# Optimization experiments

Hardware: AMD Instinct MI355X
Metric: run time of the kernel (lower is better)

The kernel has to match this reference:

```python
import jax, jax.numpy as jnp
import numpy as np

B, A, STATE_LEN, H, REL_LEN, E = 32, 64, 256, 128, 64, 16

def _mlp2(x, w1, b1, w2, b2):
    # DI-engine MLP, 2 layers, ReLU after every layer (incl. output)
    return jax.nn.relu(jax.nn.relu(x @ w1 + b1) @ w2 + b2)

def setup_inputs() -> dict:
    key = jax.random.key(0)
    ks = jax.random.split(key, 16)
    def w(k, fi, fo):
        return (jax.random.normal(k, (fi, fo), jnp.float32) / np.float32(np.sqrt(fi)))
    z = lambda n: jnp.zeros((n,), jnp.float32)
    return {
        "states": jax.random.normal(ks[0], (B, A, STATE_LEN), jnp.float32),
        "relations": jax.random.normal(ks[1], (B, A, A, REL_LEN), jnp.float32),
        "alive_mask": (jax.random.uniform(ks[2], (B, A)) > 0.3).astype(jnp.float32),
        "se_w1": w(ks[3], STATE_LEN, H), "se_b1": z(H),
        "se_w2": w(ks[4], H, H), "se_b2": z(H),
        "re_w1": w(ks[5], H + REL_LEN, H), "re_b1": z(H),
        "re_w2": w(ks[6], H, 2 * H), "re_b2": z(2 * H),
        "ra_w": w(ks[7], 3 * H, H), "ra_b": z(H),
        "ae_w1": w(ks[8], 4 * H, H), "ae_b1": z(H),
        "ae_w2": w(ks[9], H, 2 * H), "ae_b2": z(2 * H),
        "action_embed": jax.random.normal(ks[10], (E, H), jnp.float32) * np.float32(np.sqrt(2.0 / H)),
        "action_mask": jnp.ones((B, A, E + A), jnp.int32),
        "action": jax.random.randint(ks[11], (B,), 0, E + A),
        "agent_id": 0,
    }

def reference(states, relations, alive_mask,
              se_w1, se_b1, se_w2, se_b2,
              re_w1, re_b1, re_w2, re_b2,
              ra_w, ra_b,
              ae_w1, ae_b1, ae_w2, ae_b2,
              action_embed, action_mask, action, agent_id):
    del action_mask  # read by the torch module but never used
    b, a = states.shape[0], states.shape[1]
    h, e = se_w2.shape[1], action_embed.shape[0]
    # encode per-agent state: [B,A,H]
    s = _mlp2(states, se_w1, se_b1, se_w2, se_b2)
    # relation encoder: concat target-agent state onto each relation edge
    rel_in = jnp.concatenate(
        [relations, jnp.broadcast_to(s[:, None], (b, a, a, h))], axis=-1)
    r = _mlp2(rel_in, re_w1, re_b1, re_w2, re_b2)               # [B,A,A,2H]
    # relation aggregator: masked mean / masked max over source agents
    r_avr, r_max = jnp.split(r, 2, axis=-1)
    m = alive_mask[:, None, :, None]                             # [B,1,A,1]
    r_avr = (r_avr * m).mean(axis=-2)                            # [B,A,H]
    r_max = (r_max * m).max(axis=-2)                             # [B,A,H]
    s = jax.nn.relu(jnp.concatenate([s, r_avr, r_max], axis=-1) @ ra_w + ra_b)
    # pairwise action embeddings: [B,A,A,2H]
    ae_in = jnp.concatenate(
        [r,
         jnp.broadcast_to(s[:, None], (b, a, a, h)),
         jnp.broadcast_to(s[:, :, None], (b, a, a, h))], axis=-1)
    ae = _mlp2(ae_in, ae_w1, ae_b1, ae_w2, ae_b2)
    active, passive = jnp.split(ae, 2, axis=-1)                  # [B,A,A,H] each
    # acting agent `agent_id`: candidates = [embed_num self actions | A targeted actions]
    active_i = active[:, agent_id]                               # [B,A,H]
    active_full = jnp.concatenate(
        [jnp.broadcast_to(action_embed[None], (b, e, h)), active_i], axis=1)  # [B,E+A,H]
    sel = jnp.take_along_axis(active_full, action[:, None, None], axis=1)     # [B,1,H]
    state = s.at[:, agent_id].add(sel[:, 0])
    # passive side: target j receives passive embed iff action == E + j, else zero
    passive_i = passive[:, agent_id]                             # [B,A,H]
    hit = (action[:, None] == (e + jnp.arange(a))[None, :])      # [B,A]
    passive_sel = jnp.where(hit[:, :, None], passive_i, jnp.zeros((), states.dtype))
    state = state + passive_sel
    return state, sel[:, :, None], passive_sel
```

## Files before the change

### kernel.cpp

```cpp
#include <hip/hip_runtime.h>

#define NB 32
#define NA 64
#define SLEN 256
#define NH 128
#define RLEN 64
#define NE 16

typedef _Float16 f16;
typedef _Float16 f16x8 __attribute__((ext_vector_type(8)));
typedef _Float16 f16x4 __attribute__((ext_vector_type(4)));
typedef float f32x4 __attribute__((ext_vector_type(4)));

__device__ inline f16x8 cvt8(float4 a, float4 b) {
  f16x8 r;
  r[0] = (f16)a.x; r[1] = (f16)a.y; r[2] = (f16)a.z; r[3] = (f16)a.w;
  r[4] = (f16)b.x; r[5] = (f16)b.y; r[6] = (f16)b.z; r[7] = (f16)b.w;
  return r;
}

__device__ inline void gload_lds16(const float* g, float* l) {
  __builtin_amdgcn_global_load_lds((const __attribute__((address_space(1))) void*)g,
                                   (__attribute__((address_space(3))) void*)l, 16, 0, 0);
}

__global__ __launch_bounds__(256) void k0_pack(const float* __restrict__ re_w1,
                                               const float* __restrict__ re_w2,
                                               const float* __restrict__ se_w1,
                                               const float* __restrict__ se_w2,
                                               const float* __restrict__ ra_w,
                                               const float* __restrict__ ae_w1,
                                               f16* __restrict__ pk) {
  int idx = blockIdx.x * 256 + threadIdx.x;
  const float* src;
  int ro, N, ld, base;
  if (idx < 8192)        { src = re_w1; ro = 0;   N = 128; ld = 128; base = 0; }
  else if (idx < 40960)  { src = re_w2; ro = 0;   N = 256; ld = 256; base = 8192; }
  else if (idx < 73728)  { src = se_w1; ro = 0;   N = 128; ld = 128; base = 40960; }
  else if (idx < 90112)  { src = se_w2; ro = 0;   N = 128; ld = 128; base = 73728; }
  else if (idx < 106496) { src = re_w1; ro = 64;  N = 128; ld = 128; base = 90112; }
  else if (idx < 155648) { src = ra_w;  ro = 0;   N = 128; ld = 128; base = 106496; }
  else if (idx < 172032) { src = ae_w1; ro = 256; N = 128; ld = 128; base = 155648; }
  else if (idx < 188416) { src = ae_w1; ro = 384; N = 128; ld = 128; base = 172032; }
  else return;
  int li = idx - base;
  int t = li & 7, l = (li >> 3) & 63, rem = li >> 9;
  int NT = N >> 4;
  int nt = rem % NT, kt = rem / NT;
  int k = kt * 32 + (l >> 4) * 8 + t;
  int n = nt * 16 + (l & 15);
  pk[idx] = (f16)src[(size_t)(ro + k) * ld + n];
}

__global__ __launch_bounds__(256) void k1m(const float* __restrict__ states,
                                           const float* __restrict__ se_b1,
                                           const float* __restrict__ se_b2,
                                           const float* __restrict__ re_b1,
                                           const f16* __restrict__ pse1,
                                           const f16* __restrict__ pse2,
                                           const f16* __restrict__ pre1b,
                                           float* __restrict__ s_out,
                                           float* __restrict__ sproj1) {
  __shared__ f16 t1[16 * 128];
  __shared__ f16 t2[16 * 128];
  const int row0 = blockIdx.x * 16;
  const int tid = threadIdx.x;
  const int w = tid >> 6, l = tid & 63, lr = l & 15, lh = l >> 4;

  f32x4 acc[2];
  acc[0] = (f32x4){0.f, 0.f, 0.f, 0.f};
  acc[1] = (f32x4){0.f, 0.f, 0.f, 0.f};

#pragma unroll
  for (int kt = 0; kt < 8; ++kt) {
    const float* p = states + (size_t)(row0 + lr) * SLEN + kt * 32 + lh * 8;
    f16x8 aF = cvt8(*(const float4*)p, *(const float4*)(p + 4));
#pragma unroll
    for (int n = 0; n < 2; ++n) {
      f16x8 bF = *(const f16x8*)(pse1 + ((size_t)(kt * 8 + w * 2 + n) * 64 + l) * 8);
      acc[n] = __builtin_amdgcn_mfma_f32_16x16x32_f16(aF, bF, acc[n], 0, 0, 0);
    }
  }
#pragma unroll
  for (int n = 0; n < 2; ++n) {
    int h = w * 32 + n * 16 + lr;
    float bias = se_b1[h];
#pragma unroll
    for (int reg = 0; reg < 4; ++reg) {
      int j = lh * 4 + reg;
      float v = fmaxf(acc[n][reg] + bias, 0.f);
      unsigned off = (unsigned)((j * NH + h) * 2) ^ ((unsigned)(j & 7) << 4);
      *(f16*)((char*)t1 + off) = (f16)v;
    }
  }
  __syncthreads();

  acc[0] = (f32x4){0.f, 0.f, 0.f, 0.f};
  acc[1] = (f32x4){0.f, 0.f, 0.f, 0.f};
#pragma unroll
  for (int kt = 0; kt < 4; ++kt) {
    unsigned off = (unsigned)((lr * NH + kt * 32 + lh * 8) * 2) ^ ((unsigned)(lr & 7) << 4);
    f16x8 aF = *(const f16x8*)((char*)t1 + off);
#pragma unroll
    for (int n = 0; n < 2; ++n) {
      f16x8 bF = *(const f16x8*)(pse2 + ((size_t)(kt * 8 + w * 2 + n) * 64 + l) * 8);
      acc[n] = __builtin_amdgcn_mfma_f32_16x16x32_f16(aF, bF, acc[n], 0, 0, 0);
    }
  }
#pragma unroll
  for (int n = 0; n < 2; ++n) {
    int h = w * 32 + n * 16 + lr;
    float bias = se_b2[h];
#pragma unroll
    for (int reg = 0; reg < 4; ++reg) {
      int j = lh * 4 + reg;
      float v = fmaxf(acc[n][reg] + bias, 0.f);
      s_out[(size_t)(row0 + j) * NH + h] = v;
      unsigned off = (unsigned)((j * NH + h) * 2) ^ ((unsigned)(j & 7) << 4);
      *(f16*)((char*)t2 + off) = (f16)v;
    }
  }
  __syncthreads();

  acc[0] = (f32x4){0.f, 0.f, 0.f, 0.f};
  acc[1] = (f32x4){0.f, 0.f, 0.f, 0.f};
#pragma unroll
  for (int kt = 0; kt < 4; ++kt) {
    unsigned off = (unsigned)((lr * NH + kt * 32 + lh * 8) * 2) ^ ((unsigned)(lr & 7) << 4);
    f16x8 aF = *(const f16x8*)((char*)t2 + off);
#pragma unroll
    for (int n = 0; n < 2; ++n) {
      f16x8 bF = *(const f16x8*)(pre1b + ((size_t)(kt * 8 + w * 2 + n) * 64 + l) * 8);
      acc[n] = __builtin_amdgcn_mfma_f32_16x16x32_f16(aF, bF, acc[n], 0, 0, 0);
    }
  }
#pragma unroll
  for (int n = 0; n < 2; ++n) {
    int h = w * 32 + n * 16 + lr;
    float bias = re_b1[h];
#pragma unroll
    for (int reg = 0; reg < 4; ++reg) {
      int j = lh * 4 + reg;
      sproj1[(size_t)(row0 + j) * NH + h] = acc[n][reg] + bias;
    }
  }
}

__global__ __launch_bounds__(256) void k3_rel(const float* __restrict__ relations,
                                              const float* __restrict__ alive_mask,
                                              const float* __restrict__ sproj1,
                                              const float* __restrict__ re_b2,
                                              const f16* __restrict__ pw1,
                                              const f16* __restrict__ pw2,
                                              const int* __restrict__ agent_id,
                                              float* __restrict__ r_red,
                                              f16* __restrict__ r_agent) {
  __shared__ f16 tl[64 * 128];
  __shared__ float sp_lds[64 * 128];
  __shared__ float alive[NA];
  const int bid = blockIdx.x;
  const int b = bid >> 6, i = bid & 63;
  const int tid = threadIdx.x;
  const int w = tid >> 6, l = tid & 63, lr = l & 15, lh = l >> 4;

  {
    const float* spb = sproj1 + (size_t)b * NA * NH;
#pragma unroll
    for (int it = 0; it < 8; ++it) {
      int off = w * 2048 + it * 256;
      gload_lds16(spb + off + l * 4, sp_lds + off);
    }
  }
  if (tid < 64) alive[tid] = alive_mask[b * NA + tid];
  float bz[4];
#pragma unroll
  for (int n = 0; n < 4; ++n) bz[n] = re_b2[w * 64 + n * 16 + lr];

  const float* relp = relations + (size_t)bid * NA * RLEN;
  f16x8 a1[4][2];
#pragma unroll
  for (int mt = 0; mt < 4; ++mt)
#pragma unroll
    for (int kt = 0; kt < 2; ++kt) {
      const float* p = relp + (mt * 16 + lr) * RLEN + kt * 32 + lh * 8;
      a1[mt][kt] = cvt8(*(const float4*)p, *(const float4*)(p + 4));
    }
  f16x8 b1f[2][2];
#pragma unroll
  for (int kt = 0; kt < 2; ++kt)
#pragma unroll
    for (int n = 0; n < 2; ++n)
      b1f[kt][n] = *(const f16x8*)(pw1 + ((size_t)(kt * 8 + w * 2 + n) * 64 + l) * 8);

  f32x4 acc1[4][2];
#pragma unroll
  for (int mt = 0; mt < 4; ++mt)
#pragma unroll
    for (int n = 0; n < 2; ++n) acc1[mt][n] = (f32x4){0.f, 0.f, 0.f, 0.f};
#pragma unroll
  for (int kt = 0; kt < 2; ++kt)
#pragma unroll
    for (int mt = 0; mt < 4; ++mt)
#pragma unroll
      for (int n = 0; n < 2; ++n)
        acc1[mt][n] = __builtin_amdgcn_mfma_f32_16x16x32_f16(a1[mt][kt], b1f[kt][n],
                                                             acc1[mt][n], 0, 0, 0);
  __syncthreads();

#pragma unroll
  for (int mt = 0; mt < 4; ++mt)
#pragma unroll
    for (int n = 0; n < 2; ++n) {
      int h = w * 32 + n * 16 + lr;
#pragma unroll
      for (int reg = 0; reg < 4; ++reg) {
        int j = mt * 16 + lh * 4 + reg;
        float v = fmaxf(acc1[mt][n][reg] + sp_lds[j * NH + h], 0.f);
        unsigned off = (unsigned)((j * NH + h) * 2) ^ ((unsigned)(j & 7) << 4);
        *(f16*)((char*)tl + off) = (f16)v;
      }
    }
  __syncthreads();

  f32x4 acc2[4][4];
#pragma unroll
  for (int mt = 0; mt < 4; ++mt)
#pragma unroll
    for (int n = 0; n < 4; ++n) acc2[mt][n] = (f32x4){0.f, 0.f, 0.f, 0.f};
#pragma unroll
  for (int kt2 = 0; kt2 < 4; ++kt2) {
    f16x8 a2[4];
#pragma unroll
    for (int mt = 0; mt < 4; ++mt) {
      int row = mt * 16 + lr;
      unsigned off = (unsigned)((row * 256 + kt2 * 64 + lh * 16)) ^ ((unsigned)(row & 7) << 4);
      a2[mt] = *(const f16x8*)((char*)tl + off);
    }
    f16x8 b2f[4];
#pragma unroll
    for (int n = 0; n < 4; ++n)
      b2f[n] = *(const f16x8*)(pw2 + ((size_t)(kt2 * 16 + w * 4 + n) * 64 + l) * 8);
#pragma unroll
    for (int mt = 0; mt < 4; ++mt)
#pragma unroll
      for (int n = 0; n < 4; ++n)
        acc2[mt][n] = __builtin_amdgcn_mfma_f32_16x16x32_f16(a2[mt], b2f[n], acc2[mt][n], 0, 0, 0);
  }

  const int aid = agent_id[0];
  const bool isagent = (i == aid);
  const bool domax = (w >= 2);
  float red[4];
#pragma unroll
  for (int n = 0; n < 4; ++n) red[n] = 0.f;
#pragma unroll
  for (int n = 0; n < 4; ++n) {
    int col = w * 64 + n * 16 + lr;
    float bias = bz[n];
#pragma unroll
    for (int mt = 0; mt < 4; ++mt)
#pragma unroll
      for (int reg = 0; reg < 4; ++reg) {
        int j = mt * 16 + lh * 4 + reg;
        float rv = fmaxf(acc2[mt][n][reg] + bias, 0.f);
        float rm = rv * alive[j];
        red[n] = domax ? fmaxf(red[n], rm) : (red[n] + rm);
        if (isagent) r_agent[((size_t)b * NA + j) * 256 + col] = (f16)rv;
      }
  }
#pragma unroll
  for (int n = 0; n < 4; ++n) {
    float v = red[n];
    float v1 = __shfl_xor(v, 16, 64);
    v = domax ? fmaxf(v, v1) : v + v1;
    float v2 = __shfl_xor(v, 32, 64);
    v = domax ? fmaxf(v, v2) : v + v2;
    if (lh == 0) r_red[(size_t)bid * 256 + w * 64 + n * 16 + lr] = v;
  }
}

__global__ __launch_bounds__(256) void k4m(const float* __restrict__ s,
                                           const float* __restrict__ r_red,
                                           const float* __restrict__ ra_b,
                                           const f16* __restrict__ pra,
                                           const f16* __restrict__ pae1b,
                                           const f16* __restrict__ pae1c,
                                           float* __restrict__ s_new,
                                           float* __restrict__ sproj2,
                                           float* __restrict__ sproj3) {
  __shared__ f16 x3[16 * 384];
  __shared__ f16 t2[16 * 128];
  const int row0 = blockIdx.x * 16;
  const int tid = threadIdx.x;
  const int w = tid >> 6, l = tid & 63, lr = l & 15, lh = l >> 4;

#pragma unroll
  for (int it = 0; it < 6; ++it) {
    int e = it * 1024 + tid * 4;
    int row = e / 384;
    int c = e - row * 384;
    float4 v;
    if (c < 128) {
      v = *(const float4*)(s + (size_t)(row0 + row) * NH + c);
    } else {
      v = *(const float4*)(r_red + (size_t)(row0 + row) * 256 + (c - 128));
      if (c < 256) { v.x *= (1.f / 64.f); v.y *= (1.f / 64.f); v.z *= (1.f / 64.f); v.w *= (1.f / 64.f); }
    }
    f16x4 hv;
    hv[0] = (f16)v.x; hv[1] = (f16)v.y; hv[2] = (f16)v.z; hv[3] = (f16)v.w;
    unsigned off = (unsigned)((row * 384 + c) * 2) ^ ((unsigned)(row & 7) << 4);
    *(f16x4*)((char*)x3 + off) = hv;
  }
  __syncthreads();

  f32x4 acc[2];
  acc[0] = (f32x4){0.f, 0.f, 0.f, 0.f};
  acc[1] = (f32x4){0.f, 0.f, 0.f, 0.f};
#pragma unroll
  for (int kt = 0; kt < 12; ++kt) {
    unsigned off = (unsigned)((lr * 384 + kt * 32 + lh * 8) * 2) ^ ((unsigned)(lr & 7) << 4);
    f16x8 aF = *(const f16x8*)((char*)x3 + off);
#pragma unroll
    for (int n = 0; n < 2; ++n) {
      f16x8 bF = *(const f16x8*)(pra + ((size_t)(kt * 8 + w * 2 + n) * 64 + l) * 8);
      acc[n] = __builtin_amdgcn_mfma_f32_16x16x32_f16(aF, bF, acc[n], 0, 0, 0);
    }
  }
#pragma unroll
  for (int n = 0; n < 2; ++n) {
    int h = w * 32 + n * 16 + lr;
    float bias = ra_b[h];
#pragma unroll
    for (int reg = 0; reg < 4; ++reg) {
      int j = lh * 4 + reg;
      float v = fmaxf(acc[n][reg] + bias, 0.f);
      s_new[(size_t)(row0 + j) * NH + h] = v;
      unsigned off = (unsigned)((j * NH + h) * 2) ^ ((unsigned)(j & 7) << 4);
      *(f16*)((char*)t2 + off) = (f16)v;
    }
  }
  __syncthreads();

  f32x4 p2[2], p3[2];
  p2[0] = p2[1] = (f32x4){0.f, 0.f, 0.f, 0.f};
  p3[0] = p3[1] = (f32x4){0.f, 0.f, 0.f, 0.f};
#pragma unroll
  for (int kt = 0; kt < 4; ++kt) {
    unsigned off = (unsigned)((lr * NH + kt * 32 + lh * 8) * 2) ^ ((unsigned)(lr & 7) << 4);
    f16x8 aF = *(const f16x8*)((char*)t2 + off);
#pragma unroll
    for (int n = 0; n < 2; ++n) {
      f16x8 b2 = *(const f16x8*)(pae1b + ((size_t)(kt * 8 + w * 2 + n) * 64 + l) * 8);
      f16x8 b3 = *(const f16x8*)(pae1c + ((size_t)(kt * 8 + w * 2 + n) * 64 + l) * 8);
      p2[n] = __builtin_amdgcn_mfma_f32_16x16x32_f16(aF, b2, p2[n], 0, 0, 0);
      p3[n] = __builtin_amdgcn_mfma_f32_16x16x32_f16(aF, b3, p3[n], 0, 0, 0);
    }
  }
#pragma unroll
  for (int n = 0; n < 2; ++n) {
    int h = w * 32 + n * 16 + lr;
#pragma unroll
    for (int reg = 0; reg < 4; ++reg) {
      int j = lh * 4 + reg;
      sproj2[(size_t)(row0 + j) * NH + h] = p2[n][reg];
      sproj3[(size_t)(row0 + j) * NH + h] = p3[n][reg];
    }
  }
}

__global__ __launch_bounds__(256) void k5_fused(const float* __restrict__ ae_w1,
                                                const float* __restrict__ ae_b1,
                                                const float* __restrict__ ae_w2,
                                                const float* __restrict__ ae_b2,
                                                const float* __restrict__ action_embed,
                                                const int* __restrict__ action,
                                                const int* __restrict__ agent_id,
                                                const f16* __restrict__ r_agent,
                                                const float* __restrict__ sproj2,
                                                const float* __restrict__ sproj3,
                                                const float* __restrict__ s_new,
                                                float* __restrict__ out_state,
                                                float* __restrict__ out_sel,
                                                float* __restrict__ out_passive) {
  __shared__ float selL[128], pasL[128], rr[256], t[128];
  const int b = blockIdx.x;
  const int tid = threadIdx.x;
  const int h = tid & 127;
  const int act = action[b];
  const int aid = agent_id[0];

  if (act < NE) {
    if (tid < 128) {
      selL[h] = action_embed[act * NH + h];
      pasL[h] = 0.f;
    }
  } else {
    const int jj = act - NE;
    const size_t row = (size_t)b * NA + jj;
    const size_t arow = (size_t)b * NA + aid;
    rr[tid] = (float)r_agent[row * 256 + tid];
    __syncthreads();
    if (tid < 128) {
      float acc = ae_b1[h] + sproj2[row * NH + h] + sproj3[arow * NH + h];
#pragma unroll 4
      for (int k = 0; k < 256; ++k) acc += rr[k] * ae_w1[k * NH + h];
      t[h] = fmaxf(acc, 0.f);
    }
    __syncthreads();
    if (tid < 128) {
      float a_act = ae_b2[h], a_pas = ae_b2[128 + h];
#pragma unroll 4
      for (int k = 0; k < NH; ++k) {
        float tv = t[k];
        a_act += tv * ae_w2[k * 256 + h];
        a_pas += tv * ae_w2[k * 256 + 128 + h];
      }
      selL[h] = fmaxf(a_act, 0.f);
      pasL[h] = fmaxf(a_pas, 0.f);
    }
  }
  __syncthreads();
  if (tid < 128) out_sel[b * NH + h] = selL[h];

  const int prow = (act >= NE) ? (act - NE) : -1;
#pragma unroll
  for (int it = 0; it < 8; ++it) {
    int q = it * 256 + tid;
    int i = q >> 5;
    int c = (q & 31) * 4;
    size_t idx = ((size_t)b * NA + i) * NH + c;
    float4 st = *(const float4*)(s_new + idx);
    float4 ps = {0.f, 0.f, 0.f, 0.f};
    if (i == prow) {
      ps.x = pasL[c]; ps.y = pasL[c + 1]; ps.z = pasL[c + 2]; ps.w = pasL[c + 3];
      st.x += ps.x; st.y += ps.y; st.z += ps.z; st.w += ps.w;
    }
    if (i == aid) {
      st.x += selL[c]; st.y += selL[c + 1]; st.z += selL[c + 2]; st.w += selL[c + 3];
    }
    *(float4*)(out_state + idx) = st;
    *(float4*)(out_passive + idx) = ps;
  }
}

extern "C" void kernel_launch(void* const* d_in, const int* in_sizes, int n_in,
                              void* d_out, int out_size, void* d_ws, size_t ws_size,
                              hipStream_t stream) {
  (void)in_sizes; (void)n_in; (void)out_size; (void)ws_size;
  const float* states       = (const float*)d_in[0];
  const float* relations    = (const float*)d_in[1];
  const float* alive_mask   = (const float*)d_in[2];
  const float* se_w1        = (const float*)d_in[3];
  const float* se_b1        = (const float*)d_in[4];
  const float* se_w2        = (const float*)d_in[5];
  const float* se_b2        = (const float*)d_in[6];
  const float* re_w1        = (const float*)d_in[7];
  const float* re_b1        = (const float*)d_in[8];
  const float* re_w2        = (const float*)d_in[9];
  const float* re_b2        = (const float*)d_in[10];
  const float* ra_w         = (const float*)d_in[11];
  const float* ra_b         = (const float*)d_in[12];
  const float* ae_w1        = (const float*)d_in[13];
  const float* ae_b1        = (const float*)d_in[14];
  const float* ae_w2        = (const float*)d_in[15];
  const float* ae_b2        = (const float*)d_in[16];
  const float* action_embed = (const float*)d_in[17];
  const int*   action       = (const int*)d_in[19];
  const int*   agent_id     = (const int*)d_in[20];
  float* out = (float*)d_out;

  float* wsf       = (float*)d_ws;
  float* s         = wsf;
  float* sproj1    = wsf + 262144;
  float* r_red     = wsf + 524288;
  float* s_new     = wsf + 1048576;
  float* sproj2    = wsf + 1310720;
  float* sproj3    = wsf + 1572864;
  f16*   wsh       = (f16*)(wsf + 1843200);
  f16*   r_agent   = wsh;
  f16*   pk        = wsh + 524288;
  f16*   pw_re1a   = pk;
  f16*   pw_re2    = pk + 8192;
  f16*   pw_se1    = pk + 40960;
  f16*   pw_se2    = pk + 73728;
  f16*   pw_re1b   = pk + 90112;
  f16*   pw_ra     = pk + 106496;
  f16*   pw_ae1b   = pk + 155648;
  f16*   pw_ae1c   = pk + 172032;

  k0_pack<<<736, 256, 0, stream>>>(re_w1, re_w2, se_w1, se_w2, ra_w, ae_w1, pk);
  k1m<<<128, 256, 0, stream>>>(states, se_b1, se_b2, re_b1, pw_se1, pw_se2, pw_re1b,
                               s, sproj1);
  k3_rel<<<2048, 256, 0, stream>>>(relations, alive_mask, sproj1, re_b2, pw_re1a, pw_re2,
                                   agent_id, r_red, r_agent);
  k4m<<<128, 256, 0, stream>>>(s, r_red, ra_b, pw_ra, pw_ae1b, pw_ae1c,
                               s_new, sproj2, sproj3);
  k5_fused<<<32, 256, 0, stream>>>(ae_w1, ae_b1, ae_w2, ae_b2, action_embed, action,
                                   agent_id, r_agent, sproj2, sproj3, s_new,
                                   out, out + 262144, out + 266240);
}
```

Baseline: 191.4 us.

## Pack sproj1 in MFMA fragment layout and move action-embed MLP to MFMA kernel

k1m now writes sproj1 directly in the per-lane MFMA accumulator layout, so k3_rel loads it into registers with float4 reads instead of staging 32KB per block through LDS. That drops an LDS buffer and a barrier in the dominant kernel and should raise occupancy. The scalar 32-block action-embed MLP in k5_fused is replaced by a new kae kernel that runs the 2-layer MLP for all 2048 rows with f16 MFMA. A slim gather kernel then picks the needed row. This computes 64x more rows than needed and adds a kernel launch and a write of the ae_full buffer, but it removes the long serial fp32 dot-product loops.

```diff
diff --git a/kernel.cpp b/kernel.cpp
--- a/kernel.cpp
+++ b/kernel.cpp
@@ -19,17 +19,13 @@
   return r;
 }
 
-__device__ inline void gload_lds16(const float* g, float* l) {
-  __builtin_amdgcn_global_load_lds((const __attribute__((address_space(1))) void*)g,
-                                   (__attribute__((address_space(3))) void*)l, 16, 0, 0);
-}
-
 __global__ __launch_bounds__(256) void k0_pack(const float* __restrict__ re_w1,
                                                const float* __restrict__ re_w2,
                                                const float* __restrict__ se_w1,
                                                const float* __restrict__ se_w2,
                                                const float* __restrict__ ra_w,
                                                const float* __restrict__ ae_w1,
+                                               const float* __restrict__ ae_w2,
                                                f16* __restrict__ pk) {
   int idx = blockIdx.x * 256 + threadIdx.x;
   const float* src;
@@ -42,6 +38,8 @@
   else if (idx < 155648) { src = ra_w;  ro = 0;   N = 128; ld = 128; base = 106496; }
   else if (idx < 172032) { src = ae_w1; ro = 256; N = 128; ld = 128; base = 155648; }
   else if (idx < 188416) { src = ae_w1; ro = 384; N = 128; ld = 128; base = 172032; }
+  else if (idx < 221184) { src = ae_w1; ro = 0;   N = 128; ld = 128; base = 188416; }
+  else if (idx < 253952) { src = ae_w2; ro = 0;   N = 256; ld = 256; base = 221184; }
   else return;
   int li = idx - base;
   int t = li & 7, l = (li >> 3) & 63, rem = li >> 9;
@@ -60,7 +58,7 @@
                                            const f16* __restrict__ pse2,
                                            const f16* __restrict__ pre1b,
                                            float* __restrict__ s_out,
-                                           float* __restrict__ sproj1) {
+                                           float* __restrict__ sp_pk) {
   __shared__ f16 t1[16 * 128];
   __shared__ f16 t2[16 * 128];
   const int row0 = blockIdx.x * 16;
@@ -134,21 +132,22 @@
       acc[n] = __builtin_amdgcn_mfma_f32_16x16x32_f16(aF, bF, acc[n], 0, 0, 0);
     }
   }
+  const int bb = row0 >> 6;
+  const int mtile = (row0 & 63) >> 4;
 #pragma unroll
   for (int n = 0; n < 2; ++n) {
     int h = w * 32 + n * 16 + lr;
     float bias = re_b1[h];
-#pragma unroll
-    for (int reg = 0; reg < 4; ++reg) {
-      int j = lh * 4 + reg;
-      sproj1[(size_t)(row0 + j) * NH + h] = acc[n][reg] + bias;
-    }
+    float4 outv;
+#pragma unroll
+    for (int reg = 0; reg < 4; ++reg) outv[reg] = acc[n][reg] + bias;
+    *(float4*)(sp_pk + ((size_t)((bb * 4 + mtile) * 8 + w * 2 + n) * 64 + l) * 4) = outv;
   }
 }
 
 __global__ __launch_bounds__(256) void k3_rel(const float* __restrict__ relations,
                                               const float* __restrict__ alive_mask,
-                                              const float* __restrict__ sproj1,
+                                              const float* __restrict__ sp_pk,
                                               const float* __restrict__ re_b2,
                                               const f16* __restrict__ pw1,
                                               const f16* __restrict__ pw2,
@@ -156,21 +155,12 @@
                                               float* __restrict__ r_red,
                                               f16* __restrict__ r_agent) {
   __shared__ f16 tl[64 * 128];
-  __shared__ float sp_lds[64 * 128];
   __shared__ float alive[NA];
   const int bid = blockIdx.x;
   const int b = bid >> 6, i = bid & 63;
   const int tid = threadIdx.x;
   const int w = tid >> 6, l = tid & 63, lr = l & 15, lh = l >> 4;
 
-  {
-    const float* spb = sproj1 + (size_t)b * NA * NH;
-#pragma unroll
-    for (int it = 0; it < 8; ++it) {
-      int off = w * 2048 + it * 256;
-      gload_lds16(spb + off + l * 4, sp_lds + off);
-    }
-  }
   if (tid < 64) alive[tid] = alive_mask[b * NA + tid];
   float bz[4];
 #pragma unroll
@@ -191,6 +181,15 @@
 #pragma unroll
     for (int n = 0; n < 2; ++n)
       b1f[kt][n] = *(const f16x8*)(pw1 + ((size_t)(kt * 8 + w * 2 + n) * 64 + l) * 8);
+  float4 sp4[4][2];
+  {
+    const float* spp = sp_pk + (size_t)b * 8192;
+#pragma unroll
+    for (int mt = 0; mt < 4; ++mt)
+#pragma unroll
+      for (int n = 0; n < 2; ++n)
+        sp4[mt][n] = *(const float4*)(spp + (size_t)((mt * 8 + w * 2 + n) * 64 + l) * 4);
+  }
 
   f32x4 acc1[4][2];
 #pragma unroll
@@ -205,7 +204,6 @@
       for (int n = 0; n < 2; ++n)
         acc1[mt][n] = __builtin_amdgcn_mfma_f32_16x16x32_f16(a1[mt][kt], b1f[kt][n],
                                                              acc1[mt][n], 0, 0, 0);
-  __syncthreads();
 
 #pragma unroll
   for (int mt = 0; mt < 4; ++mt)
@@ -215,7 +213,7 @@
 #pragma unroll
       for (int reg = 0; reg < 4; ++reg) {
         int j = mt * 16 + lh * 4 + reg;
-        float v = fmaxf(acc1[mt][n][reg] + sp_lds[j * NH + h], 0.f);
+        float v = fmaxf(acc1[mt][n][reg] + sp4[mt][n][reg], 0.f);
         unsigned off = (unsigned)((j * NH + h) * 2) ^ ((unsigned)(j & 7) << 4);
         *(f16*)((char*)tl + off) = (f16)v;
       }
@@ -368,59 +366,103 @@
   }
 }
 
-__global__ __launch_bounds__(256) void k5_fused(const float* __restrict__ ae_w1,
-                                                const float* __restrict__ ae_b1,
-                                                const float* __restrict__ ae_w2,
-                                                const float* __restrict__ ae_b2,
-                                                const float* __restrict__ action_embed,
-                                                const int* __restrict__ action,
-                                                const int* __restrict__ agent_id,
-                                                const f16* __restrict__ r_agent,
-                                                const float* __restrict__ sproj2,
-                                                const float* __restrict__ sproj3,
-                                                const float* __restrict__ s_new,
-                                                float* __restrict__ out_state,
-                                                float* __restrict__ out_sel,
-                                                float* __restrict__ out_passive) {
-  __shared__ float selL[128], pasL[128], rr[256], t[128];
+__global__ __launch_bounds__(256) void kae(const f16* __restrict__ r_agent,
+                                           const float* __restrict__ sproj2,
+                                           const float* __restrict__ sproj3,
+                                           const float* __restrict__ ae_b1,
+                                           const float* __restrict__ ae_b2,
+                                           const f16* __restrict__ pae1a,
+                                           const f16* __restrict__ pae2,
+                                           const int* __restrict__ agent_id,
+                                           float* __restrict__ ae_full) {
+  __shared__ f16 t1[16 * 128];
+  const int row0 = blockIdx.x * 16;
+  const int b = row0 >> 6;
+  const int tid = threadIdx.x;
+  const int w = tid >> 6, l = tid & 63, lr = l & 15, lh = l >> 4;
+  const int aid = agent_id[0];
+
+  f32x4 acc[2];
+  acc[0] = (f32x4){0.f, 0.f, 0.f, 0.f};
+  acc[1] = (f32x4){0.f, 0.f, 0.f, 0.f};
+#pragma unroll
+  for (int kt = 0; kt < 8; ++kt) {
+    f16x8 aF = *(const f16x8*)(r_agent + (size_t)(row0 + lr) * 256 + kt * 32 + lh * 8);
+#pragma unroll
+    for (int n = 0; n < 2; ++n) {
+      f16x8 bF = *(const f16x8*)(pae1a + ((size_t)(kt * 8 + w * 2 + n) * 64 + l) * 8);
+      acc[n] = __builtin_amdgcn_mfma_f32_16x16x32_f16(aF, bF, acc[n], 0, 0, 0);
+    }
+  }
+#pragma unroll
+  for (int n = 0; n < 2; ++n) {
+    int h = w * 32 + n * 16 + lr;
+    float base = ae_b1[h] + sproj3[((size_t)b * NA + aid) * NH + h];
+#pragma unroll
+    for (int reg = 0; reg < 4; ++reg) {
+      int j = lh * 4 + reg;
+      float v = fmaxf(acc[n][reg] + base + sproj2[(size_t)(row0 + j) * NH + h], 0.f);
+      unsigned off = (unsigned)((j * NH + h) * 2) ^ ((unsigned)(j & 7) << 4);
+      *(f16*)((char*)t1 + off) = (f16)v;
+    }
+  }
+  __syncthreads();
+
+  f32x4 acc2[4];
+#pragma unroll
+  for (int n = 0; n < 4; ++n) acc2[n] = (f32x4){0.f, 0.f, 0.f, 0.f};
+#pragma unroll
+  for (int kt = 0; kt < 4; ++kt) {
+    unsigned off = (unsigned)((lr * NH + kt * 32 + lh * 8) * 2) ^ ((unsigned)(lr & 7) << 4);
+    f16x8 aF = *(const f16x8*)((char*)t1 + off);
+#pragma unroll
+    for (int n = 0; n < 4; ++n) {
+      f16x8 bF = *(const f16x8*)(pae2 + ((size_t)(kt * 16 + w * 4 + n) * 64 + l) * 8);
+      acc2[n] = __builtin_amdgcn_mfma_f32_16x16x32_f16(aF, bF, acc2[n], 0, 0, 0);
+    }
+  }
+#pragma unroll
+  for (int n = 0; n < 4; ++n) {
+    int col = w * 64 + n * 16 + lr;
+    float bias = ae_b2[col];
+#pragma unroll
+    for (int reg = 0; reg < 4; ++reg) {
+      int j = lh * 4 + reg;
+      ae_full[(size_t)(row0 + j) * 256 + col] = fmaxf(acc2[n][reg] + bias, 0.f);
+    }
+  }
+}
+
+__global__ __launch_bounds__(256) void k5g(const float* __restrict__ action_embed,
+                                           const int* __restrict__ action,
+                                           const int* __restrict__ agent_id,
+                                           const float* __restrict__ ae_full,
+                                           const float* __restrict__ s_new,
+                                           float* __restrict__ out_state,
+                                           float* __restrict__ out_sel,
+                                           float* __restrict__ out_passive) {
+  __shared__ float selL[128], pasL[128];
   const int b = blockIdx.x;
   const int tid = threadIdx.x;
   const int h = tid & 127;
   const int act = action[b];
   const int aid = agent_id[0];
 
-  if (act < NE) {
-    if (tid < 128) {
-      selL[h] = action_embed[act * NH + h];
-      pasL[h] = 0.f;
-    }
-  } else {
-    const int jj = act - NE;
-    const size_t row = (size_t)b * NA + jj;
-    const size_t arow = (size_t)b * NA + aid;
-    rr[tid] = (float)r_agent[row * 256 + tid];
-    __syncthreads();
-    if (tid < 128) {
-      float acc = ae_b1[h] + sproj2[row * NH + h] + sproj3[arow * NH + h];
-#pragma unroll 4
-      for (int k = 0; k < 256; ++k) acc += rr[k] * ae_w1[k * NH + h];
-      t[h] = fmaxf(acc, 0.f);
-    }
-    __syncthreads();
-    if (tid < 128) {
-      float a_act = ae_b2[h], a_pas = ae_b2[128 + h];
-#pragma unroll 4
-      for (int k = 0; k < NH; ++k) {
-        float tv = t[k];
-        a_act += tv * ae_w2[k * 256 + h];
-        a_pas += tv * ae_w2[k * 256 + 128 + h];
-      }
-      selL[h] = fmaxf(a_act, 0.f);
-      pasL[h] = fmaxf(a_pas, 0.f);
-    }
-  }
-  __syncthreads();
-  if (tid < 128) out_sel[b * NH + h] = selL[h];
+  if (tid < 128) {
+    float sv, pv;
+    if (act < NE) {
+      sv = action_embed[act * NH + h];
+      pv = 0.f;
+    } else {
+      size_t r = (size_t)(b * NA + act - NE) * 256;
+      sv = ae_full[r + h];
+      pv = ae_full[r + 128 + h];
+    }
+    selL[h] = sv;
+    pasL[h] = pv;
+    out_sel[b * NH + h] = sv;
+  }
+  __syncthreads();
 
   const int prow = (act >= NE) ? (act - NE) : -1;
 #pragma unroll
@@ -469,33 +511,37 @@
   const int*   agent_id     = (const int*)d_in[20];
   float* out = (float*)d_out;
 
-  float* wsf       = (float*)d_ws;
-  float* s         = wsf;
-  float* sproj1    = wsf + 262144;
-  float* r_red     = wsf + 524288;
-  float* s_new     = wsf + 1048576;
-  float* sproj2    = wsf + 1310720;
-  float* sproj3    = wsf + 1572864;
-  f16*   wsh       = (f16*)(wsf + 1843200);
-  f16*   r_agent   = wsh;
-  f16*   pk        = wsh + 524288;
-  f16*   pw_re1a   = pk;
-  f16*   pw_re2    = pk + 8192;
-  f16*   pw_se1    = pk + 40960;
-  f16*   pw_se2    = pk + 73728;
-  f16*   pw_re1b   = pk + 90112;
-  f16*   pw_ra     = pk + 106496;
-  f16*   pw_ae1b   = pk + 155648;
-  f16*   pw_ae1c   = pk + 172032;
-
-  k0_pack<<<736, 256, 0, stream>>>(re_w1, re_w2, se_w1, se_w2, ra_w, ae_w1, pk);
+  float* wsf     = (float*)d_ws;
+  float* s       = wsf;
+  float* sp_pk   = wsf + 262144;
+  float* r_red   = wsf + 524288;
+  float* s_new   = wsf + 1048576;
+  float* sproj2  = wsf + 1310720;
+  float* sproj3  = wsf + 1572864;
+  float* ae_full = wsf + 1835008;
+  f16*   wsh     = (f16*)(wsf + 2359296);
+  f16*   r_agent = wsh;
+  f16*   pk      = wsh + 524288;
+  f16*   pw_re1a = pk;
+  f16*   pw_re2  = pk + 8192;
+  f16*   pw_se1  = pk + 40960;
+  f16*   pw_se2  = pk + 73728;
+  f16*   pw_re1b = pk + 90112;
+  f16*   pw_ra   = pk + 106496;
+  f16*   pw_ae1b = pk + 155648;
+  f16*   pw_ae1c = pk + 172032;
+  f16*   pw_ae1a = pk + 188416;
+  f16*   pw_ae2  = pk + 221184;
+
+  k0_pack<<<992, 256, 0, stream>>>(re_w1, re_w2, se_w1, se_w2, ra_w, ae_w1, ae_w2, pk);
   k1m<<<128, 256, 0, stream>>>(states, se_b1, se_b2, re_b1, pw_se1, pw_se2, pw_re1b,
-                               s, sproj1);
-  k3_rel<<<2048, 256, 0, stream>>>(relations, alive_mask, sproj1, re_b2, pw_re1a, pw_re2,
+                               s, sp_pk);
+  k3_rel<<<2048, 256, 0, stream>>>(relations, alive_mask, sp_pk, re_b2, pw_re1a, pw_re2,
                                    agent_id, r_red, r_agent);
   k4m<<<128, 256, 0, stream>>>(s, r_red, ra_b, pw_ra, pw_ae1b, pw_ae1c,
                                s_new, sproj2, sproj3);
-  k5_fused<<<32, 256, 0, stream>>>(ae_w1, ae_b1, ae_w2, ae_b2, action_embed, action,
-                                   agent_id, r_agent, sproj2, sproj3, s_new,
-                                   out, out + 262144, out + 266240);
-}
+  kae<<<128, 256, 0, stream>>>(r_agent, sproj2, sproj3, ae_b1, ae_b2, pw_ae1a, pw_ae2,
+                               agent_id, ae_full);
+  k5g<<<32, 256, 0, stream>>>(action_embed, action, agent_id, ae_full, s_new,
+                              out, out + 262144, out + 266240);
+}
```

New measurement: 167.6 us. 12.4% less time.
